# Kernel tuning notes

Hardware: AMD Instinct MI355X
Metric: run time of the kernel (lower is better)

## Reference

```python
import jax, jax.numpy as jnp
import numpy as np

M, K, N = 32, 8192, 8192      # tokens, infeatures, outfeatures
GROUP = 128                   # quantization group size along K
PACK = 8                      # 32 bits / 4 bits per value


def _dequant(qweight, scales):
    """Unpack int4 nibbles (packed 8-per-int32 along K) and apply per-group
    symmetric dequant: w = (q - 8) * scale, matching Marlin's fused dequant."""
    kp, n = qweight.shape  # (K//8, N)
    shifts = (4 * jnp.arange(PACK, dtype=jnp.int32))[None, :, None]
    q = ((qweight[:, None, :] >> shifts) & 15)          # (K//8, 8, N)
    q = q.reshape(kp * PACK, n).astype(jnp.float32)     # (K, N)
    groups = scales.shape[0]
    gsz = (kp * PACK) // groups
    w = (q.reshape(groups, gsz, n) - 8.0) * scales[:, None, :]
    return w.reshape(kp * PACK, n)                      # (K, N) fp


def setup_inputs() -> dict:
    key = jax.random.key(0)
    kA, kQ, kS, kB = jax.random.split(key, 4)
    A = jax.random.normal(kA, (M, K), jnp.float32)
    # draw raw 4-bit codes then pack 8 of them into each int32 along K
    q4 = jax.random.randint(kQ, (K, N), 0, 16, jnp.int32)
    shifts = (4 * jnp.arange(PACK, dtype=jnp.int32))[None, :, None]
    qweight = jnp.sum(q4.reshape(K // PACK, PACK, N) << shifts, axis=1).astype(jnp.int32)
    scales = jax.random.uniform(kS, (K // GROUP, N), jnp.float32, 0.005, 0.02)
    bias = jax.random.normal(kB, (N,), jnp.float32) * 0.01
    return {"A": A, "qweight": qweight, "scales": scales, "bias": bias}


def reference(A, qweight, scales, bias):
    # Marlin mul(A, B, C, s) computes C = A @ dequant(B, s); then + bias
    W = _dequant(qweight, scales)          # (K, N)
    return A @ W + bias                    # (M, N)
```

## Files before the change

kernel.cpp:

```cpp
#include <hip/hip_runtime.h>
#include <hip/hip_bf16.h>
#include <stdint.h>

#define M_DIM 32
#define K_DIM 8192
#define N_DIM 8192
#define NGROUPS 64
#define KSPLIT 16
#define KPART (K_DIM / KSPLIT)
#define GPART (NGROUPS / KSPLIT)
#define BN 128

typedef __attribute__((ext_vector_type(8))) short short8;
typedef __attribute__((ext_vector_type(4))) float floatx4;

#define AS1(p) ((const __attribute__((address_space(1))) void*)(p))
#define AS3(p) ((__attribute__((address_space(3))) void*)(p))

__global__ void marlin_prep_kernel(const float* __restrict__ A,
                                   uint16_t* __restrict__ Abf,
                                   float* __restrict__ R,
                                   float4* __restrict__ out4) {
    const int m = blockIdx.x;
    const int qtr = blockIdx.y;
    const int t = threadIdx.x;
    const int octet = qtr * 256 + t;
    const int k0 = octet * 8;

    {
        const int gtid = (qtr * 32 + m) * 256 + t;
        const float4 z = make_float4(0.f, 0.f, 0.f, 0.f);
        out4[gtid * 2] = z;
        out4[gtid * 2 + 1] = z;
    }

    const float* a = A + m * K_DIM + k0;
    uint16_t b[8];
    float sum = 0.f;
#pragma unroll
    for (int j = 0; j < 8; j++) {
        union { __hip_bfloat16 h; uint16_t u; } cv;
        cv.h = __float2bfloat16(a[j]);
        b[j] = cv.u;
        sum += __bfloat162float(cv.h);
    }
    uint32_t w0 = (uint32_t)b[0] | ((uint32_t)b[4] << 16);
    uint32_t w1 = (uint32_t)b[1] | ((uint32_t)b[5] << 16);
    uint32_t w2 = (uint32_t)b[2] | ((uint32_t)b[6] << 16);
    uint32_t w3 = (uint32_t)b[3] | ((uint32_t)b[7] << 16);
    *(uint4*)(Abf + (size_t)m * K_DIM + k0) = make_uint4(w0, w1, w2, w3);

#pragma unroll
    for (int off = 1; off < 16; off <<= 1) sum += __shfl_xor(sum, off, 16);
    if ((t & 15) == 0) R[m * NGROUPS + qtr * 16 + (t >> 4)] = sum;
}

__global__ __launch_bounds__(512, 4) void
MarlinQuantLinear_68556267979256_kernel(const int* __restrict__ qw,
                                        const float* __restrict__ scales,
                                        const float* __restrict__ bias,
                                        const uint16_t* __restrict__ Abf,
                                        const float* __restrict__ R,
                                        float* __restrict__ out) {
    __shared__ uint32_t qbuf[2][16 * 128];
    __shared__ uint32_t abuf[2][32 * 64];
    __shared__ float    r_lds[32 * 5];

    const int bx = blockIdx.x;
    const int bz = blockIdx.y;
    const int nbase = bx * BN;
    const int kbase = bz * KPART;
    const int gbase = bz * GPART;
    const int qrow0 = bz * (KPART / 8);

    const int tid = threadIdx.x;
    const int w = tid >> 6;
    const int lane = tid & 63;
    const int quad = lane >> 4;
    const int l16 = lane & 15;
    const int mtile = w & 1;
    const int nt0 = (w >> 1) * 2;
    const int ncol0 = nbase + nt0 * 16 + l16;
    const int ncol1 = ncol0 + 16;
    const int arow = mtile * 16 + l16;

    if (tid < 128) {
        const int mm = tid >> 2, gg = tid & 3;
        r_lds[mm * 5 + gg] = 136.0f * R[mm * NGROUPS + gbase + gg];
    }

    const float* scol = scales + (size_t)gbase * N_DIM;
    float s0[GPART], s1[GPART];
#pragma unroll
    for (int g = 0; g < GPART; g++) {
        s0[g] = scol[g * N_DIM + ncol0];
        s1[g] = scol[g * N_DIM + ncol1];
    }

    const int sra = tid >> 4, spa = tid & 15;
    const uint16_t* ga_base = Abf + (size_t)sra * K_DIM + kbase
                            + ((spa ^ (sra & 15)) << 3);
    const int srq = tid >> 5, spq = tid & 31;
    const int* gq_base = qw + (size_t)(qrow0 + srq) * N_DIM + nbase
                       + ((spq * 4) ^ ((srq & 1) << 4));

    auto stage = [&](int g, int buf) {
        __builtin_amdgcn_global_load_lds(AS1(ga_base + g * 128),
                                         AS3(&abuf[buf][w * 256]), 16, 0, 0);
        __builtin_amdgcn_global_load_lds(AS1(gq_base + (size_t)g * 16 * N_DIM),
                                         AS3(&qbuf[buf][w * 256]), 16, 0, 0);
    };

    stage(0, 0);

    floatx4 C0 = {0.f, 0.f, 0.f, 0.f};
    floatx4 C1 = {0.f, 0.f, 0.f, 0.f};

#pragma unroll
    for (int g = 0; g < GPART; g++) {
        __syncthreads();
        if (g + 1 < GPART) stage(g + 1, (g + 1) & 1);

        const uint32_t* qb = qbuf[g & 1];
        const uint32_t* ab = abuf[g & 1];
        floatx4 acc0 = {0.f, 0.f, 0.f, 0.f};
        floatx4 acc1 = {0.f, 0.f, 0.f, 0.f};
#pragma unroll
        for (int t = 0; t < 4; t++) {
            const int qrow = (t * 4 + quad) * 128;
            const uint32_t qA =
                qb[qrow + ((nt0 * 16 + l16) ^ ((quad & 1) << 4))];
            const uint32_t qB =
                qb[qrow + (((nt0 + 1) * 16 + l16) ^ ((quad & 1) << 4))];
            const short8 fa = *(const short8*)
                &ab[arow * 64 + (((t * 4 + quad) ^ (arow & 15)) << 2)];
            union { uint32_t u[4]; short8 v; } fb;
            fb.u[0] = ( qA        & 0x000F000Fu) | 0x43004300u;
            fb.u[1] = ((qA >> 4)  & 0x000F000Fu) | 0x43004300u;
            fb.u[2] = ((qA >> 8)  & 0x000F000Fu) | 0x43004300u;
            fb.u[3] = ((qA >> 12) & 0x000F000Fu) | 0x43004300u;
            acc0 = __builtin_amdgcn_mfma_f32_16x16x32_bf16(fa, fb.v, acc0, 0, 0, 0);
            fb.u[0] = ( qB        & 0x000F000Fu) | 0x43004300u;
            fb.u[1] = ((qB >> 4)  & 0x000F000Fu) | 0x43004300u;
            fb.u[2] = ((qB >> 8)  & 0x000F000Fu) | 0x43004300u;
            fb.u[3] = ((qB >> 12) & 0x000F000Fu) | 0x43004300u;
            acc1 = __builtin_amdgcn_mfma_f32_16x16x32_bf16(fa, fb.v, acc1, 0, 0, 0);
        }
#pragma unroll
        for (int r = 0; r < 4; r++) {
            const float Rv = r_lds[(mtile * 16 + quad * 4 + r) * 5 + g];
            C0[r] = fmaf(s0[g], acc0[r] - Rv, C0[r]);
            C1[r] = fmaf(s1[g], acc1[r] - Rv, C1[r]);
        }
    }

    const float bv0 = (bz == 0) ? bias[ncol0] : 0.0f;
    const float bv1 = (bz == 0) ? bias[ncol1] : 0.0f;
#pragma unroll
    for (int r = 0; r < 4; r++) {
        const int m = mtile * 16 + quad * 4 + r;
        atomicAdd(&out[(size_t)m * N_DIM + ncol0], C0[r] + bv0);
        atomicAdd(&out[(size_t)m * N_DIM + ncol1], C1[r] + bv1);
    }
}

extern "C" void kernel_launch(void* const* d_in, const int* in_sizes, int n_in,
                              void* d_out, int out_size, void* d_ws, size_t ws_size,
                              hipStream_t stream) {
    const float* A      = (const float*)d_in[0];
    const int*   qw     = (const int*)d_in[1];
    const float* scales = (const float*)d_in[2];
    const float* bias   = (const float*)d_in[3];
    float* out = (float*)d_out;

    uint16_t* Abf = (uint16_t*)d_ws;
    float*    R   = (float*)((char*)d_ws + (size_t)M_DIM * K_DIM * 2);

    marlin_prep_kernel<<<dim3(M_DIM, 4), 256, 0, stream>>>(A, Abf, R, (float4*)out);
    MarlinQuantLinear_68556267979256_kernel<<<dim3(N_DIM / BN, KSPLIT), 512, 0, stream>>>(
        qw, scales, bias, Abf, R, out);
}
```

Before: 94.26 us.

## Fuse activation bf16 conversion into GEMM and replace atomics with split-K reduce kernel

Removes the separate prep kernel: each GEMM block loads its fp32 A slice, converts it to bf16 into LDS, and computes the per-group row sums itself, with one column of blocks writing them out. Split-K partials are written to a workspace and summed by a new reduce kernel that also applies the zero-point correction (scale times row sum) and the bias, replacing the global atomics. The qweight staging changes from async global-to-LDS double buffering to register prefetch with two barriers per group. In exchange, every block re-converts A redundantly, there is extra partial-buffer traffic of about 16 MB, and the per-group loads now pass through registers.

```diff
diff --git a/kernel.cpp b/kernel.cpp
--- a/kernel.cpp
+++ b/kernel.cpp
@@ -14,57 +14,23 @@
 typedef __attribute__((ext_vector_type(8))) short short8;
 typedef __attribute__((ext_vector_type(4))) float floatx4;
 
-#define AS1(p) ((const __attribute__((address_space(1))) void*)(p))
-#define AS3(p) ((__attribute__((address_space(3))) void*)(p))
-
-__global__ void marlin_prep_kernel(const float* __restrict__ A,
-                                   uint16_t* __restrict__ Abf,
-                                   float* __restrict__ R,
-                                   float4* __restrict__ out4) {
-    const int m = blockIdx.x;
-    const int qtr = blockIdx.y;
-    const int t = threadIdx.x;
-    const int octet = qtr * 256 + t;
-    const int k0 = octet * 8;
-
-    {
-        const int gtid = (qtr * 32 + m) * 256 + t;
-        const float4 z = make_float4(0.f, 0.f, 0.f, 0.f);
-        out4[gtid * 2] = z;
-        out4[gtid * 2 + 1] = z;
-    }
-
-    const float* a = A + m * K_DIM + k0;
-    uint16_t b[8];
-    float sum = 0.f;
-#pragma unroll
-    for (int j = 0; j < 8; j++) {
-        union { __hip_bfloat16 h; uint16_t u; } cv;
-        cv.h = __float2bfloat16(a[j]);
-        b[j] = cv.u;
-        sum += __bfloat162float(cv.h);
-    }
-    uint32_t w0 = (uint32_t)b[0] | ((uint32_t)b[4] << 16);
-    uint32_t w1 = (uint32_t)b[1] | ((uint32_t)b[5] << 16);
-    uint32_t w2 = (uint32_t)b[2] | ((uint32_t)b[6] << 16);
-    uint32_t w3 = (uint32_t)b[3] | ((uint32_t)b[7] << 16);
-    *(uint4*)(Abf + (size_t)m * K_DIM + k0) = make_uint4(w0, w1, w2, w3);
-
-#pragma unroll
-    for (int off = 1; off < 16; off <<= 1) sum += __shfl_xor(sum, off, 16);
-    if ((t & 15) == 0) R[m * NGROUPS + qtr * 16 + (t >> 4)] = sum;
+static __device__ __forceinline__ uint32_t bf16bits(float x) {
+    union { __hip_bfloat16 h; uint16_t u; } cv;
+    cv.h = __float2bfloat16(x);
+    return (uint32_t)cv.u;
+}
+static __device__ __forceinline__ float bf16val(float x) {
+    return __bfloat162float(__float2bfloat16(x));
 }
 
 __global__ __launch_bounds__(512, 4) void
 MarlinQuantLinear_68556267979256_kernel(const int* __restrict__ qw,
                                         const float* __restrict__ scales,
-                                        const float* __restrict__ bias,
-                                        const uint16_t* __restrict__ Abf,
-                                        const float* __restrict__ R,
-                                        float* __restrict__ out) {
-    __shared__ uint32_t qbuf[2][16 * 128];
-    __shared__ uint32_t abuf[2][32 * 64];
-    __shared__ float    r_lds[32 * 5];
+                                        const float* __restrict__ A,
+                                        float* __restrict__ P,
+                                        float* __restrict__ Rws) {
+    __shared__ uint32_t abuf[32 * 256];
+    __shared__ uint32_t qbuf[16 * 128];
 
     const int bx = blockIdx.x;
     const int bz = blockIdx.y;
@@ -84,10 +50,9 @@
     const int ncol1 = ncol0 + 16;
     const int arow = mtile * 16 + l16;
 
-    if (tid < 128) {
-        const int mm = tid >> 2, gg = tid & 3;
-        r_lds[mm * 5 + gg] = 136.0f * R[mm * NGROUPS + gbase + gg];
-    }
+    const int qr = tid >> 5, qc = tid & 31;
+    const int* qsrc = qw + (size_t)(qrow0 + qr) * N_DIM + nbase + qc * 4;
+    uint4 qreg = *(const uint4*)qsrc;
 
     const float* scol = scales + (size_t)gbase * N_DIM;
     float s0[GPART], s1[GPART];
@@ -97,43 +62,70 @@
         s1[g] = scol[g * N_DIM + ncol1];
     }
 
-    const int sra = tid >> 4, spa = tid & 15;
-    const uint16_t* ga_base = Abf + (size_t)sra * K_DIM + kbase
-                            + ((spa ^ (sra & 15)) << 3);
-    const int srq = tid >> 5, spq = tid & 31;
-    const int* gq_base = qw + (size_t)(qrow0 + srq) * N_DIM + nbase
-                       + ((spq * 4) ^ ((srq & 1) << 4));
-
-    auto stage = [&](int g, int buf) {
-        __builtin_amdgcn_global_load_lds(AS1(ga_base + g * 128),
-                                         AS3(&abuf[buf][w * 256]), 16, 0, 0);
-        __builtin_amdgcn_global_load_lds(AS1(gq_base + (size_t)g * 16 * N_DIM),
-                                         AS3(&qbuf[buf][w * 256]), 16, 0, 0);
-    };
-
-    stage(0, 0);
+    const int srow = tid >> 4, sseg = tid & 15;
+    const float4* af4 = (const float4*)(A + (size_t)srow * K_DIM + kbase);
+    float4 f4[8];
+#pragma unroll
+    for (int j = 0; j < 8; j++) f4[j] = af4[sseg + 16 * j];
+
+    uint32_t own[8][4];
+    float rpart[GPART];
+#pragma unroll
+    for (int g = 0; g < GPART; g++) rpart[g] = 0.f;
+#pragma unroll
+    for (int j = 0; j < 8; j++) {
+        own[j][0] = bf16bits(f4[j].x); own[j][1] = bf16bits(f4[j].y);
+        own[j][2] = bf16bits(f4[j].z); own[j][3] = bf16bits(f4[j].w);
+        rpart[j >> 1] += bf16val(f4[j].x) + bf16val(f4[j].y)
+                       + bf16val(f4[j].z) + bf16val(f4[j].w);
+    }
+#pragma unroll
+    for (int j = 0; j < 8; j++) {
+        float nx = __shfl_xor(f4[j].x, 1), ny = __shfl_xor(f4[j].y, 1);
+        float nz = __shfl_xor(f4[j].z, 1), nw = __shfl_xor(f4[j].w, 1);
+        if ((sseg & 1) == 0) {
+            uint32_t w0 = own[j][0] | (bf16bits(nx) << 16);
+            uint32_t w1 = own[j][1] | (bf16bits(ny) << 16);
+            uint32_t w2 = own[j][2] | (bf16bits(nz) << 16);
+            uint32_t w3 = own[j][3] | (bf16bits(nw) << 16);
+            const int o = (sseg >> 1) + 8 * j;
+            const int pos = o ^ (srow & 15);
+            *(uint4*)&abuf[srow * 256 + pos * 4] = make_uint4(w0, w1, w2, w3);
+        }
+    }
+#pragma unroll
+    for (int g = 0; g < GPART; g++) {
+#pragma unroll
+        for (int off = 1; off < 16; off <<= 1)
+            rpart[g] += __shfl_xor(rpart[g], off);
+    }
+    if (bx == 0 && sseg == 0) {
+#pragma unroll
+        for (int g = 0; g < GPART; g++)
+            Rws[srow * NGROUPS + gbase + g] = 136.0f * rpart[g];
+    }
+
+    const int qdst = qr * 128 + (qc ^ ((qr & 1) << 2)) * 4;
+    *(uint4*)&qbuf[qdst] = qreg;
+    qreg = *(const uint4*)(qsrc + (size_t)16 * N_DIM);
+    __syncthreads();
 
     floatx4 C0 = {0.f, 0.f, 0.f, 0.f};
     floatx4 C1 = {0.f, 0.f, 0.f, 0.f};
 
 #pragma unroll
     for (int g = 0; g < GPART; g++) {
-        __syncthreads();
-        if (g + 1 < GPART) stage(g + 1, (g + 1) & 1);
-
-        const uint32_t* qb = qbuf[g & 1];
-        const uint32_t* ab = abuf[g & 1];
         floatx4 acc0 = {0.f, 0.f, 0.f, 0.f};
         floatx4 acc1 = {0.f, 0.f, 0.f, 0.f};
 #pragma unroll
         for (int t = 0; t < 4; t++) {
             const int qrow = (t * 4 + quad) * 128;
-            const uint32_t qA =
-                qb[qrow + ((nt0 * 16 + l16) ^ ((quad & 1) << 4))];
-            const uint32_t qB =
-                qb[qrow + (((nt0 + 1) * 16 + l16) ^ ((quad & 1) << 4))];
+            const int swz = (quad & 1) << 4;
+            const uint32_t qA = qbuf[qrow + (ncol0 - nbase ^ swz)];
+            const uint32_t qB = qbuf[qrow + (ncol1 - nbase ^ swz)];
+            const int c = g * 16 + t * 4 + quad;
             const short8 fa = *(const short8*)
-                &ab[arow * 64 + (((t * 4 + quad) ^ (arow & 15)) << 2)];
+                &abuf[arow * 256 + (c ^ (arow & 15)) * 4];
             union { uint32_t u[4]; short8 v; } fb;
             fb.u[0] = ( qA        & 0x000F000Fu) | 0x43004300u;
             fb.u[1] = ((qA >> 4)  & 0x000F000Fu) | 0x43004300u;
@@ -148,19 +140,63 @@
         }
 #pragma unroll
         for (int r = 0; r < 4; r++) {
-            const float Rv = r_lds[(mtile * 16 + quad * 4 + r) * 5 + g];
-            C0[r] = fmaf(s0[g], acc0[r] - Rv, C0[r]);
-            C1[r] = fmaf(s1[g], acc1[r] - Rv, C1[r]);
-        }
-    }
-
-    const float bv0 = (bz == 0) ? bias[ncol0] : 0.0f;
-    const float bv1 = (bz == 0) ? bias[ncol1] : 0.0f;
+            C0[r] = fmaf(s0[g], acc0[r], C0[r]);
+            C1[r] = fmaf(s1[g], acc1[r], C1[r]);
+        }
+        if (g + 1 < GPART) {
+            __syncthreads();
+            *(uint4*)&qbuf[qdst] = qreg;
+            if (g + 2 < GPART)
+                qreg = *(const uint4*)(qsrc + (size_t)(g + 2) * 16 * N_DIM);
+            __syncthreads();
+        }
+    }
+
 #pragma unroll
     for (int r = 0; r < 4; r++) {
         const int m = mtile * 16 + quad * 4 + r;
-        atomicAdd(&out[(size_t)m * N_DIM + ncol0], C0[r] + bv0);
-        atomicAdd(&out[(size_t)m * N_DIM + ncol1], C1[r] + bv1);
+        P[((size_t)bz * 32 + m) * N_DIM + ncol0] = C0[r];
+        P[((size_t)bz * 32 + m) * N_DIM + ncol1] = C1[r];
+    }
+}
+
+__global__ void marlin_reduce_kernel(const float* __restrict__ P,
+                                     const float* __restrict__ Rws,
+                                     const float* __restrict__ scales,
+                                     const float* __restrict__ bias,
+                                     float* __restrict__ out) {
+    __shared__ float s_l[64 * 64];
+    __shared__ float r_l[32 * 64];
+    const int tid = threadIdx.x;
+    const int nblk = blockIdx.x * 64;
+#pragma unroll
+    for (int i = 0; i < 16; i++) {
+        const int idx = i * 256 + tid;
+        s_l[idx] = scales[(size_t)(idx >> 6) * N_DIM + nblk + (idx & 63)];
+    }
+#pragma unroll
+    for (int i = 0; i < 8; i++) {
+        const int idx = i * 256 + tid;
+        r_l[idx] = Rws[idx];
+    }
+    __syncthreads();
+
+    const int c = tid & 63;
+    const int mq = tid >> 6;
+    const int n = nblk + c;
+    const float bv = bias[n];
+#pragma unroll
+    for (int mi = 0; mi < 8; mi++) {
+        const int m = mq * 8 + mi;
+        float acc = bv;
+#pragma unroll
+        for (int bz = 0; bz < KSPLIT; bz++)
+            acc += P[((size_t)bz * 32 + m) * N_DIM + n];
+        float corr = 0.f;
+#pragma unroll
+        for (int g = 0; g < NGROUPS; g++)
+            corr = fmaf(s_l[g * 64 + c], r_l[m * 64 + g], corr);
+        out[(size_t)m * N_DIM + n] = acc - corr;
     }
 }
 
@@ -173,10 +209,10 @@
     const float* bias   = (const float*)d_in[3];
     float* out = (float*)d_out;
 
-    uint16_t* Abf = (uint16_t*)d_ws;
-    float*    R   = (float*)((char*)d_ws + (size_t)M_DIM * K_DIM * 2);
-
-    marlin_prep_kernel<<<dim3(M_DIM, 4), 256, 0, stream>>>(A, Abf, R, (float4*)out);
+    float* P   = (float*)d_ws;
+    float* Rws = (float*)((char*)d_ws + (size_t)16 * 1024 * 1024);
+
     MarlinQuantLinear_68556267979256_kernel<<<dim3(N_DIM / BN, KSPLIT), 512, 0, stream>>>(
-        qw, scales, bias, Abf, R, out);
-}
+        qw, scales, A, P, Rws);
+    marlin_reduce_kernel<<<128, 256, 0, stream>>>(P, Rws, scales, bias, out);
+}
```

Result: slower. 101.5 us (+7.7%).
